# Kernel optimization log

Measured on AMD Instinct MI355X. Metric: run time of the kernel, lower is better.

The kernel has to match this reference:

```python
import jax, jax.numpy as jnp
import numpy as np

BETA = 0.25

def setup_inputs() -> dict:
    key = jax.random.key(0)
    k1, k2 = jax.random.split(key)
    x = jax.random.normal(k1, (32, 1024, 256), dtype=jnp.float32)
    # tf.random_uniform_initializer default range is [-0.05, 0.05)
    embedding = jax.random.uniform(k2, (256, 8192), dtype=jnp.float32, minval=-0.05, maxval=0.05)
    return {"x": x, "embedding": embedding}


def reference(x, embedding):
    # x: [B, S, D]; embedding: [D, K] (codebook stored column-wise, as in the tf module)
    D = x.shape[-1]
    flat = x.reshape(-1, D)                                   # [N, D]
    dists = (jnp.sum(flat * flat, axis=1, keepdims=True)
             - 2.0 * (flat @ embedding)
             + jnp.sum(embedding * embedding, axis=0))
    idx = jnp.argmin(dists, axis=1)                           # [N] int
    quantized = jnp.take(embedding.T, idx, axis=0).reshape(x.shape)  # gather codebook columns
    # VQ losses
    commitment = jnp.mean(jnp.square(jax.lax.stop_gradient(quantized) - x))
    codebook = jnp.mean(jnp.square(quantized - jax.lax.stop_gradient(x)))
    loss = BETA * commitment + codebook
    # straight-through estimator
    quantized_st = x + jax.lax.stop_gradient(quantized - x)
    return quantized_st, loss
```

## Files before the change

### kernel.cpp

```cpp
#include <hip/hip_runtime.h>

typedef float f4   __attribute__((ext_vector_type(4)));
typedef float f2   __attribute__((ext_vector_type(2)));
typedef _Float16 f16x8 __attribute__((ext_vector_type(8)));
typedef float f32x4  __attribute__((ext_vector_type(4)));

#define N_ROWS  32768
#define D_DIM   256
#define K_CODES 8192
#define NUM_ELEM (N_ROWS * D_DIM)
#define EPS_MARGIN 2e-3f
#define FB_CAP  8192
#define FB_RPB  8
#define RF_SLICES 16
#define N_PANELS 256
#define HALF_PANELS 128

__device__ __forceinline__ void gl2lds16(const void* g, void* l) {
    __builtin_amdgcn_global_load_lds(
        (const __attribute__((address_space(1))) unsigned int*)g,
        (__attribute__((address_space(3))) unsigned int*)l, 16, 0, 0);
}

__global__ void prep_kernel(const float* __restrict__ E, short* __restrict__ Ep,
                            float* __restrict__ Et32, float* __restrict__ ee) {
    __shared__ float eepart[8][32];
    const int p  = blockIdx.x;
    const int t  = threadIdx.x;
    const int c  = t & 31;
    const int gq = t >> 5;
    const int cp = p * 32;
    short* ph = Ep + (size_t)p * 8192;
    float ss = 0.0f;
    #pragma unroll
    for (int gi = 0; gi < 4; ++gi) {
        int g = gq * 4 + gi;
        f16x8 h;
        f4 av, bv;
        #pragma unroll
        for (int j = 0; j < 8; ++j) {
            float v = E[(size_t)(g * 8 + j) * K_CODES + cp + c];
            h[j] = (_Float16)v;
            ss += v * v;
            if (j < 4) av[j] = v; else bv[j - 4] = v;
        }
        *(f16x8*)(ph + (g * 32 + c) * 8) = h;
        *(f4*)(Et32 + (size_t)(cp + c) * D_DIM + g * 8)     = av;
        *(f4*)(Et32 + (size_t)(cp + c) * D_DIM + g * 8 + 4) = bv;
    }
    eepart[gq][c] = ss;
    __syncthreads();
    if (t < 32) {
        float s = 0.0f;
        #pragma unroll
        for (int q = 0; q < 8; ++q) s += eepart[q][t];
        ee[cp + t] = s;
    }
}

__launch_bounds__(256, 2)
__global__ void mfma_sieve_kernel(const float* __restrict__ X,
                                  const short* __restrict__ Ep,
                                  const float* __restrict__ ee,
                                  f2* __restrict__ res_bs,
                                  int* __restrict__ res_idx) {
    __shared__ __align__(16) short Bbuf[2][8192];
    const int t    = threadIdx.x;
    const int w    = t >> 6;
    const int lane = t & 63;
    const int n    = lane & 15;
    const int quad = lane >> 4;
    const int half = blockIdx.x & 1;
    const int row0 = (blockIdx.x >> 1) * 128;
    const int rw   = row0 + w * 32;
    const int p0   = half * HALF_PANELS;

    f16x8 Ah[2][8];
    #pragma unroll
    for (int rt = 0; rt < 2; ++rt) {
        const float* xp = X + (size_t)(rw + rt * 16 + n) * D_DIM;
        #pragma unroll
        for (int ks = 0; ks < 8; ++ks) {
            int d = ks * 32 + quad * 8;
            f4 a = *(const f4*)(xp + d);
            f4 b = *(const f4*)(xp + d + 4);
            f16x8 h;
            #pragma unroll
            for (int j = 0; j < 8; ++j) {
                float x = (j < 4) ? a[j] : b[j - 4];
                h[j] = (_Float16)x;
            }
            Ah[rt][ks] = h;
        }
    }

    float bestv[8], secv[8]; int besti[8];
    #pragma unroll
    for (int s = 0; s < 8; ++s) { bestv[s] = 1e30f; secv[s] = 1e30f; besti[s] = 0; }

    {
        const char* gp = (const char*)Ep + (size_t)p0 * 16384;
        char* lp = (char*)&Bbuf[0][0];
        #pragma unroll
        for (int i = 0; i < 4; ++i)
            gl2lds16(gp + (w * 4 + i) * 1024 + lane * 16, lp + (w * 4 + i) * 1024);
    }
    __syncthreads();

    for (int i = 0; i < HALF_PANELS; ++i) {
        const int p   = p0 + i;
        const int buf = i & 1;
        if (i + 1 < HALF_PANELS) {
            const char* gp = (const char*)Ep + (size_t)(p + 1) * 16384;
            char* lp = (char*)&Bbuf[buf ^ 1][0];
            #pragma unroll
            for (int k = 0; k < 4; ++k)
                gl2lds16(gp + (w * 4 + k) * 1024 + lane * 16, lp + (w * 4 + k) * 1024);
        }

        const short* Bh = &Bbuf[buf][0];

        f32x4 acc[2][2];
        #pragma unroll
        for (int ct = 0; ct < 2; ++ct)
            #pragma unroll
            for (int rt = 0; rt < 2; ++rt)
                acc[ct][rt] = (f32x4)(0.0f);

        #pragma unroll
        for (int ks = 0; ks < 8; ++ks) {
            const int g = ks * 4 + quad;
            f16x8 bh[2];
            #pragma unroll
            for (int ct = 0; ct < 2; ++ct) {
                int c = ct * 16 + n;
                bh[ct] = *(const f16x8*)(Bh + (g * 32 + c) * 8);
            }
            #pragma unroll
            for (int ct = 0; ct < 2; ++ct)
                #pragma unroll
                for (int rt = 0; rt < 2; ++rt)
                    acc[ct][rt] = __builtin_amdgcn_mfma_f32_16x16x32_f16(Ah[rt][ks], bh[ct], acc[ct][rt], 0, 0, 0);
        }

        const int cb = p * 32;
        #pragma unroll
        for (int ct = 0; ct < 2; ++ct) {
            int code = cb + ct * 16 + n;
            float eev = ee[code];
            #pragma unroll
            for (int rt = 0; rt < 2; ++rt)
                #pragma unroll
                for (int r = 0; r < 4; ++r) {
                    float key = fmaf(-2.0f, acc[ct][rt][r], eev);
                    int s = rt * 4 + r;
                    float nb = fminf(key, bestv[s]);
                    secv[s]  = fminf(secv[s], fmaxf(key, bestv[s]));
                    besti[s] = (key < bestv[s]) ? code : besti[s];
                    bestv[s] = nb;
                }
        }
        __syncthreads();
    }

    #pragma unroll
    for (int off = 1; off < 16; off <<= 1) {
        #pragma unroll
        for (int s = 0; s < 8; ++s) {
            float ov = __shfl_xor(bestv[s], off);
            int   oi = __shfl_xor(besti[s], off);
            float os = __shfl_xor(secv[s], off);
            bool owin = (ov < bestv[s]) || (ov == bestv[s] && oi < besti[s]);
            if (owin) { secv[s] = fminf(os, bestv[s]); bestv[s] = ov; besti[s] = oi; }
            else      { secv[s] = fminf(secv[s], ov); }
        }
    }

    if (n == 0) {
        #pragma unroll
        for (int s = 0; s < 8; ++s) {
            int rl  = w * 32 + (s >> 2) * 16 + quad * 4 + (s & 3);
            int row = row0 + rl;
            f2 bs; bs[0] = bestv[s]; bs[1] = secv[s];
            res_bs[(size_t)row * 2 + half]  = bs;
            res_idx[(size_t)row * 2 + half] = besti[s];
        }
    }
}

__global__ void gather_kernel(const float* __restrict__ X, const float* __restrict__ Et32,
                              const f2* __restrict__ res_bs, const int* __restrict__ res_idx,
                              int* __restrict__ counter, int2* __restrict__ list,
                              float* __restrict__ out, double* __restrict__ loss_sum) {
    __shared__ int bl_[128];
    const int t    = threadIdx.x;
    const int row0 = blockIdx.x * 128;
    if (t < 128) {
        const int row = row0 + t;
        f2 a = res_bs[(size_t)row * 2];
        f2 b = res_bs[(size_t)row * 2 + 1];
        int ia = res_idx[(size_t)row * 2];
        int ib = res_idx[(size_t)row * 2 + 1];
        float gb; int gi; float gs;
        if (b[0] < a[0]) { gb = b[0]; gi = ib; gs = fminf(b[1], a[0]); }
        else             { gb = a[0]; gi = ia; gs = fminf(a[1], b[0]); }
        bl_[t] = gi;
        if (gs - gb <= EPS_MARGIN) {
            int pos = atomicAdd(counter, 1);
            if (pos < FB_CAP) list[pos] = make_int2(row, gi);
        }
    }
    __syncthreads();
    double ls = 0.0;
    const int d = t;
    #pragma unroll 4
    for (int r = 0; r < 128; ++r) {
        int code = bl_[r];
        float q  = Et32[(size_t)code * D_DIM + d];
        float x  = X[(size_t)(row0 + r) * D_DIM + d];
        float dq = q - x;
        out[(size_t)(row0 + r) * D_DIM + d] = x + dq;
        ls += (double)dq * (double)dq;
    }
    #pragma unroll
    for (int off = 32; off > 0; off >>= 1)
        ls += __shfl_down(ls, off);
    if ((t & 63) == 0) atomicAdd(loss_sum, ls);
}

__global__ void refine1_kernel(const float* __restrict__ X, const float* __restrict__ E,
                               const int* __restrict__ counter, const int2* __restrict__ list,
                               double* __restrict__ res_v, int* __restrict__ res_i) {
    __shared__ float xt[D_DIM][FB_RPB];
    __shared__ int rows_sh[FB_RPB];
    __shared__ double wbv[4][FB_RPB];
    __shared__ int    wbi[4][FB_RPB];

    int nf = *counter; if (nf > FB_CAP) nf = FB_CAP;
    const int nchunks = (nf + FB_RPB - 1) / FB_RPB;
    const int nitems  = nchunks * RF_SLICES;
    const int t = threadIdx.x;

    for (int item = blockIdx.x; item < nitems; item += gridDim.x) {
        const int rc = item / RF_SLICES;
        const int sl = item % RF_SLICES;
        __syncthreads();
        if (t < FB_RPB) {
            int e = rc * FB_RPB + t;
            int2 ent = list[(e < nf) ? e : 0];
            rows_sh[t] = ent.x;
        }
        __syncthreads();
        #pragma unroll
        for (int j = 0; j < FB_RPB; ++j)
            xt[t][j] = X[(size_t)rows_sh[j] * D_DIM + t];
        __syncthreads();

        const int k0 = sl * 512 + t * 2;
        double s0[FB_RPB], s1[FB_RPB], q0 = 0.0, q1 = 0.0;
        #pragma unroll
        for (int j = 0; j < FB_RPB; ++j) { s0[j] = 0.0; s1[j] = 0.0; }
        for (int d = 0; d < D_DIM; ++d) {
            f2 ev = *(const f2*)(E + (size_t)d * K_CODES + k0);
            double e0d = (double)ev[0], e1d = (double)ev[1];
            const f4* xp = (const f4*)(&xt[d][0]);
            f4 xa = xp[0], xb = xp[1];
            double xd[FB_RPB] = { (double)xa[0], (double)xa[1], (double)xa[2], (double)xa[3],
                                  (double)xb[0], (double)xb[1], (double)xb[2], (double)xb[3] };
            q0 += e0d * e0d; q1 += e1d * e1d;
            #pragma unroll
            for (int j = 0; j < FB_RPB; ++j) {
                s0[j] += xd[j] * e0d;
                s1[j] += xd[j] * e1d;
            }
        }
        double bv[FB_RPB]; int bi[FB_RPB];
        #pragma unroll
        for (int j = 0; j < FB_RPB; ++j) {
            double k0v = q0 - 2.0 * s0[j];
            double k1v = q1 - 2.0 * s1[j];
            bv[j] = k0v; bi[j] = k0;
            if (k1v < bv[j]) { bv[j] = k1v; bi[j] = k0 + 1; }
        }
        #pragma unroll
        for (int off = 1; off < 64; off <<= 1) {
            #pragma unroll
            for (int j = 0; j < FB_RPB; ++j) {
                double ov = __shfl_xor(bv[j], off);
                int    oi = __shfl_xor(bi[j], off);
                if (ov < bv[j] || (ov == bv[j] && oi < bi[j])) { bv[j] = ov; bi[j] = oi; }
            }
        }
        const int wave = t >> 6;
        if ((t & 63) == 0) {
            #pragma unroll
            for (int j = 0; j < FB_RPB; ++j) { wbv[wave][j] = bv[j]; wbi[wave][j] = bi[j]; }
        }
        __syncthreads();
        if (t < FB_RPB) {
            double b = wbv[0][t]; int i_ = wbi[0][t];
            #pragma unroll
            for (int wv = 1; wv < 4; ++wv) {
                double ov = wbv[wv][t]; int oi = wbi[wv][t];
                if (ov < b || (ov == b && oi < i_)) { b = ov; i_ = oi; }
            }
            int e = rc * FB_RPB + t;
            res_v[(size_t)e * RF_SLICES + sl] = b;
            res_i[(size_t)e * RF_SLICES + sl] = i_;
        }
    }
}

__global__ void patch_kernel(const float* __restrict__ X, const float* __restrict__ Et32,
                             float* __restrict__ out, double* __restrict__ loss_sum,
                             const int* __restrict__ counter, const int2* __restrict__ list,
                             const double* __restrict__ res_v, const int* __restrict__ res_i) {
    int nf = *counter; if (nf > FB_CAP) nf = FB_CAP;
    const int b = blockIdx.x;
    if (b >= nf) return;
    __shared__ int nc_sh;
    const int t = threadIdx.x;
    if (t == 0) {
        double bv = res_v[(size_t)b * RF_SLICES]; int bi = res_i[(size_t)b * RF_SLICES];
        for (int s = 1; s < RF_SLICES; ++s) {
            double v = res_v[(size_t)b * RF_SLICES + s];
            int    i = res_i[(size_t)b * RF_SLICES + s];
            if (v < bv || (v == bv && i < bi)) { bv = v; bi = i; }
        }
        nc_sh = bi;
    }
    __syncthreads();
    int2 ent = list[b];
    const int oc = ent.y, row = ent.x, nc = nc_sh;
    if (nc == oc) return;
    float x  = X[(size_t)row * D_DIM + t];
    float qn = Et32[(size_t)nc * D_DIM + t];
    float qo = Et32[(size_t)oc * D_DIM + t];
    float dqn = qn - x, dqo = qo - x;
    out[(size_t)row * D_DIM + t] = x + dqn;
    double dl = (double)dqn * dqn - (double)dqo * dqo;
    #pragma unroll
    for (int off = 32; off > 0; off >>= 1)
        dl += __shfl_down(dl, off);
    if ((t & 63) == 0) atomicAdd(loss_sum, dl);
}

__global__ void fin_kernel(const double* __restrict__ loss_sum, float* __restrict__ out) {
    double m = loss_sum[0] / (double)NUM_ELEM;
    out[NUM_ELEM] = (float)(0.25 * m + m);
}

extern "C" void kernel_launch(void* const* d_in, const int* in_sizes, int n_in,
                              void* d_out, int out_size, void* d_ws, size_t ws_size,
                              hipStream_t stream) {
    const float* X = (const float*)d_in[0];
    const float* E = (const float*)d_in[1];
    float* out = (float*)d_out;

    double* loss_sum = (double*)d_ws;
    int*    counter  = (int*)((char*)d_ws + 8);
    float*  ee       = (float*)((char*)d_ws + 1024);
    int2*   list     = (int2*)((char*)d_ws + 36864);
    double* res_v    = (double*)((char*)d_ws + 131072);
    int*    res_i    = (int*)((char*)d_ws + 1179648);
    float*  Et32     = (float*)((char*)d_ws + 1703936);
    short*  Ep       = (short*)((char*)d_ws + 10092544);
    f2*     res_bs   = (f2*)((char*)d_ws + 14286848);
    int*    res_idx  = (int*)((char*)d_ws + 15335424);

    hipMemsetAsync(d_ws, 0, 1024, stream);
    prep_kernel<<<N_PANELS, 256, 0, stream>>>(E, Ep, Et32, ee);
    mfma_sieve_kernel<<<512, 256, 0, stream>>>(X, Ep, ee, res_bs, res_idx);
    gather_kernel<<<N_ROWS / 128, 256, 0, stream>>>(X, Et32, res_bs, res_idx,
                                                    counter, list, out, loss_sum);
    refine1_kernel<<<2048, 256, 0, stream>>>(X, E, counter, list, res_v, res_i);
    patch_kernel<<<FB_CAP, 256, 0, stream>>>(X, Et32, out, loss_sum, counter, list,
                                             res_v, res_i);
    fin_kernel<<<1, 1, 0, stream>>>(loss_sum, out);
}
```

Before: 326.1 us.

## Fuse refine, patch and finalize via last-block atomics; fold ee into MFMA accumulator

```diff
diff --git a/kernel.cpp b/kernel.cpp
--- a/kernel.cpp
+++ b/kernel.cpp
@@ -23,13 +23,20 @@
 }
 
 __global__ void prep_kernel(const float* __restrict__ E, short* __restrict__ Ep,
-                            float* __restrict__ Et32, float* __restrict__ ee) {
+                            float* __restrict__ Et32, float* __restrict__ ee,
+                            float* __restrict__ ctl) {
     __shared__ float eepart[8][32];
     const int p  = blockIdx.x;
     const int t  = threadIdx.x;
     const int c  = t & 31;
     const int gq = t >> 5;
     const int cp = p * 32;
+    if (p == 0) {
+        f4 z = (f4)(0.0f);
+        f4* dst = (f4*)ctl;
+        dst[t * 2]     = z;
+        dst[t * 2 + 1] = z;
+    }
     short* ph = Ep + (size_t)p * 8192;
     float ss = 0.0f;
     #pragma unroll
@@ -65,6 +72,7 @@
                                   f2* __restrict__ res_bs,
                                   int* __restrict__ res_idx) {
     __shared__ __align__(16) short Bbuf[2][8192];
+    __shared__ float eebuf[4096];
     const int t    = threadIdx.x;
     const int w    = t >> 6;
     const int lane = t & 63;
@@ -94,9 +102,17 @@
         }
     }
 
+    {
+        const f4* src = (const f4*)(ee + half * 4096);
+        f4* dst = (f4*)eebuf;
+        #pragma unroll
+        for (int ps = 0; ps < 4; ++ps)
+            dst[ps * 256 + t] = src[ps * 256 + t];
+    }
+
     float bestv[8], secv[8]; int besti[8];
     #pragma unroll
-    for (int s = 0; s < 8; ++s) { bestv[s] = 1e30f; secv[s] = 1e30f; besti[s] = 0; }
+    for (int s = 0; s < 8; ++s) { bestv[s] = -1e30f; secv[s] = -1e30f; besti[s] = 0; }
 
     {
         const char* gp = (const char*)Ep + (size_t)p0 * 16384;
@@ -119,13 +135,16 @@
         }
 
         const short* Bh = &Bbuf[buf][0];
-
+        const int po = i * 32;
+
+        float eh0 = -0.5f * eebuf[po + n];
+        float eh1 = -0.5f * eebuf[po + 16 + n];
         f32x4 acc[2][2];
         #pragma unroll
-        for (int ct = 0; ct < 2; ++ct)
-            #pragma unroll
-            for (int rt = 0; rt < 2; ++rt)
-                acc[ct][rt] = (f32x4)(0.0f);
+        for (int rt = 0; rt < 2; ++rt) {
+            #pragma unroll
+            for (int r = 0; r < 4; ++r) { acc[0][rt][r] = eh0; acc[1][rt][r] = eh1; }
+        }
 
         #pragma unroll
         for (int ks = 0; ks < 8; ++ks) {
@@ -147,16 +166,15 @@
         #pragma unroll
         for (int ct = 0; ct < 2; ++ct) {
             int code = cb + ct * 16 + n;
-            float eev = ee[code];
             #pragma unroll
             for (int rt = 0; rt < 2; ++rt)
                 #pragma unroll
                 for (int r = 0; r < 4; ++r) {
-                    float key = fmaf(-2.0f, acc[ct][rt][r], eev);
+                    float av = acc[ct][rt][r];
                     int s = rt * 4 + r;
-                    float nb = fminf(key, bestv[s]);
-                    secv[s]  = fminf(secv[s], fmaxf(key, bestv[s]));
-                    besti[s] = (key < bestv[s]) ? code : besti[s];
+                    float nb = fmaxf(av, bestv[s]);
+                    secv[s]  = fmaxf(secv[s], fminf(av, bestv[s]));
+                    besti[s] = (av > bestv[s]) ? code : besti[s];
                     bestv[s] = nb;
                 }
         }
@@ -170,9 +188,9 @@
             float ov = __shfl_xor(bestv[s], off);
             int   oi = __shfl_xor(besti[s], off);
             float os = __shfl_xor(secv[s], off);
-            bool owin = (ov < bestv[s]) || (ov == bestv[s] && oi < besti[s]);
-            if (owin) { secv[s] = fminf(os, bestv[s]); bestv[s] = ov; besti[s] = oi; }
-            else      { secv[s] = fminf(secv[s], ov); }
+            bool owin = (ov > bestv[s]) || (ov == bestv[s] && oi < besti[s]);
+            if (owin) { secv[s] = fmaxf(os, bestv[s]); bestv[s] = ov; besti[s] = oi; }
+            else      { secv[s] = fmaxf(secv[s], ov); }
         }
     }
 
@@ -181,7 +199,7 @@
         for (int s = 0; s < 8; ++s) {
             int rl  = w * 32 + (s >> 2) * 16 + quad * 4 + (s & 3);
             int row = row0 + rl;
-            f2 bs; bs[0] = bestv[s]; bs[1] = secv[s];
+            f2 bs; bs[0] = -2.0f * bestv[s]; bs[1] = -2.0f * secv[s];
             res_bs[(size_t)row * 2 + half]  = bs;
             res_idx[(size_t)row * 2 + half] = besti[s];
         }
@@ -228,18 +246,31 @@
     if ((t & 63) == 0) atomicAdd(loss_sum, ls);
 }
 
-__global__ void refine1_kernel(const float* __restrict__ X, const float* __restrict__ E,
-                               const int* __restrict__ counter, const int2* __restrict__ list,
-                               double* __restrict__ res_v, int* __restrict__ res_i) {
+__global__ void refine_kernel(const float* __restrict__ X, const float* __restrict__ E,
+                              const float* __restrict__ Et32, float* __restrict__ out,
+                              double* __restrict__ loss_sum,
+                              const int* __restrict__ counter, const int2* __restrict__ list,
+                              double* __restrict__ res_v, int* __restrict__ res_i,
+                              int* __restrict__ chunk_done, int* __restrict__ done_chunks) {
     __shared__ float xt[D_DIM][FB_RPB];
     __shared__ int rows_sh[FB_RPB];
     __shared__ double wbv[4][FB_RPB];
     __shared__ int    wbi[4][FB_RPB];
+    __shared__ int nc_sh[FB_RPB];
+    __shared__ int last_sh;
 
     int nf = *counter; if (nf > FB_CAP) nf = FB_CAP;
     const int nchunks = (nf + FB_RPB - 1) / FB_RPB;
     const int nitems  = nchunks * RF_SLICES;
     const int t = threadIdx.x;
+
+    if (nitems == 0) {
+        if (blockIdx.x == 0 && t == 0) {
+            double m = loss_sum[0] / (double)NUM_ELEM;
+            out[NUM_ELEM] = (float)(0.25 * m + m);
+        }
+        return;
+    }
 
     for (int item = blockIdx.x; item < nitems; item += gridDim.x) {
         const int rc = item / RF_SLICES;
@@ -308,46 +339,65 @@
             res_v[(size_t)e * RF_SLICES + sl] = b;
             res_i[(size_t)e * RF_SLICES + sl] = i_;
         }
-    }
-}
-
-__global__ void patch_kernel(const float* __restrict__ X, const float* __restrict__ Et32,
-                             float* __restrict__ out, double* __restrict__ loss_sum,
-                             const int* __restrict__ counter, const int2* __restrict__ list,
-                             const double* __restrict__ res_v, const int* __restrict__ res_i) {
-    int nf = *counter; if (nf > FB_CAP) nf = FB_CAP;
-    const int b = blockIdx.x;
-    if (b >= nf) return;
-    __shared__ int nc_sh;
-    const int t = threadIdx.x;
-    if (t == 0) {
-        double bv = res_v[(size_t)b * RF_SLICES]; int bi = res_i[(size_t)b * RF_SLICES];
-        for (int s = 1; s < RF_SLICES; ++s) {
-            double v = res_v[(size_t)b * RF_SLICES + s];
-            int    i = res_i[(size_t)b * RF_SLICES + s];
-            if (v < bv || (v == bv && i < bi)) { bv = v; bi = i; }
-        }
-        nc_sh = bi;
-    }
-    __syncthreads();
-    int2 ent = list[b];
-    const int oc = ent.y, row = ent.x, nc = nc_sh;
-    if (nc == oc) return;
-    float x  = X[(size_t)row * D_DIM + t];
-    float qn = Et32[(size_t)nc * D_DIM + t];
-    float qo = Et32[(size_t)oc * D_DIM + t];
-    float dqn = qn - x, dqo = qo - x;
-    out[(size_t)row * D_DIM + t] = x + dqn;
-    double dl = (double)dqn * dqn - (double)dqo * dqo;
-    #pragma unroll
-    for (int off = 32; off > 0; off >>= 1)
-        dl += __shfl_down(dl, off);
-    if ((t & 63) == 0) atomicAdd(loss_sum, dl);
-}
-
-__global__ void fin_kernel(const double* __restrict__ loss_sum, float* __restrict__ out) {
-    double m = loss_sum[0] / (double)NUM_ELEM;
-    out[NUM_ELEM] = (float)(0.25 * m + m);
+
+        __threadfence();
+        __syncthreads();
+        if (t == 0) {
+            int old = atomicAdd(&chunk_done[rc], 1);
+            last_sh = (old == RF_SLICES - 1) ? 1 : 0;
+        }
+        __syncthreads();
+        if (last_sh) {
+            __threadfence();
+            if (t < FB_RPB) {
+                int e = rc * FB_RPB + t;
+                int nc = -1;
+                if (e < nf) {
+                    double bv_ = atomicAdd(&res_v[(size_t)e * RF_SLICES], 0.0);
+                    int    bi_ = atomicOr(&res_i[(size_t)e * RF_SLICES], 0);
+                    for (int s = 1; s < RF_SLICES; ++s) {
+                        double v  = atomicAdd(&res_v[(size_t)e * RF_SLICES + s], 0.0);
+                        int    i_ = atomicOr(&res_i[(size_t)e * RF_SLICES + s], 0);
+                        if (v < bv_ || (v == bv_ && i_ < bi_)) { bv_ = v; bi_ = i_; }
+                    }
+                    nc = bi_;
+                }
+                nc_sh[t] = nc;
+            }
+            __syncthreads();
+            double dl = 0.0;
+            #pragma unroll
+            for (int j = 0; j < FB_RPB; ++j) {
+                int e = rc * FB_RPB + j;
+                if (e < nf) {
+                    int nc = nc_sh[j];
+                    int2 ent = list[e];
+                    if (nc != ent.y) {
+                        float x  = xt[t][j];
+                        float qn = Et32[(size_t)nc * D_DIM + t];
+                        float qo = Et32[(size_t)ent.y * D_DIM + t];
+                        float dqn = qn - x, dqo = qo - x;
+                        out[(size_t)ent.x * D_DIM + t] = x + dqn;
+                        dl += (double)dqn * dqn - (double)dqo * dqo;
+                    }
+                }
+            }
+            #pragma unroll
+            for (int off = 32; off > 0; off >>= 1)
+                dl += __shfl_down(dl, off);
+            if ((t & 63) == 0 && dl != 0.0) atomicAdd(loss_sum, dl);
+            __threadfence();
+            __syncthreads();
+            if (t == 0) {
+                int oldc = atomicAdd(done_chunks, 1);
+                if (oldc == nchunks - 1) {
+                    __threadfence();
+                    double m = atomicAdd(loss_sum, 0.0) / (double)NUM_ELEM;
+                    out[NUM_ELEM] = (float)(0.25 * m + m);
+                }
+            }
+        }
+    }
 }
 
 extern "C" void kernel_launch(void* const* d_in, const int* in_sizes, int n_in,
@@ -357,24 +407,23 @@
     const float* E = (const float*)d_in[1];
     float* out = (float*)d_out;
 
-    double* loss_sum = (double*)d_ws;
-    int*    counter  = (int*)((char*)d_ws + 8);
-    float*  ee       = (float*)((char*)d_ws + 1024);
-    int2*   list     = (int2*)((char*)d_ws + 36864);
-    double* res_v    = (double*)((char*)d_ws + 131072);
-    int*    res_i    = (int*)((char*)d_ws + 1179648);
-    float*  Et32     = (float*)((char*)d_ws + 1703936);
-    short*  Ep       = (short*)((char*)d_ws + 10092544);
-    f2*     res_bs   = (f2*)((char*)d_ws + 14286848);
-    int*    res_idx  = (int*)((char*)d_ws + 15335424);
-
-    hipMemsetAsync(d_ws, 0, 1024, stream);
-    prep_kernel<<<N_PANELS, 256, 0, stream>>>(E, Ep, Et32, ee);
+    double* loss_sum    = (double*)d_ws;
+    int*    counter     = (int*)((char*)d_ws + 8);
+    int*    done_chunks = (int*)((char*)d_ws + 16);
+    int*    chunk_done  = (int*)((char*)d_ws + 64);
+    float*  ee          = (float*)((char*)d_ws + 8192);
+    int2*   list        = (int2*)((char*)d_ws + 40960);
+    double* res_v       = (double*)((char*)d_ws + 131072);
+    int*    res_i       = (int*)((char*)d_ws + 1179648);
+    float*  Et32        = (float*)((char*)d_ws + 1703936);
+    short*  Ep          = (short*)((char*)d_ws + 10092544);
+    f2*     res_bs      = (f2*)((char*)d_ws + 14286848);
+    int*    res_idx     = (int*)((char*)d_ws + 15335424);
+
+    prep_kernel<<<N_PANELS, 256, 0, stream>>>(E, Ep, Et32, ee, (float*)d_ws);
     mfma_sieve_kernel<<<512, 256, 0, stream>>>(X, Ep, ee, res_bs, res_idx);
     gather_kernel<<<N_ROWS / 128, 256, 0, stream>>>(X, Et32, res_bs, res_idx,
                                                     counter, list, out, loss_sum);
-    refine1_kernel<<<2048, 256, 0, stream>>>(X, E, counter, list, res_v, res_i);
-    patch_kernel<<<FB_CAP, 256, 0, stream>>>(X, Et32, out, loss_sum, counter, list,
-                                             res_v, res_i);
-    fin_kernel<<<1, 1, 0, stream>>>(loss_sum, out);
-}
+    refine_kernel<<<2048, 256, 0, stream>>>(X, E, Et32, out, loss_sum, counter, list,
+                                            res_v, res_i, chunk_done, done_chunks);
+}
```

Measured after the change: 408.3 us. 25.2% more time.

## Restructure fp64 refine kernel, fold workspace memset into prep, grid-stride patch

Applied to the files above, without the earlier changes.

```diff
diff --git a/kernel.cpp b/kernel.cpp
--- a/kernel.cpp
+++ b/kernel.cpp
@@ -11,8 +11,8 @@
 #define NUM_ELEM (N_ROWS * D_DIM)
 #define EPS_MARGIN 2e-3f
 #define FB_CAP  8192
-#define FB_RPB  8
-#define RF_SLICES 16
+#define FB_RPB  16
+#define RF_SLICES 32
 #define N_PANELS 256
 #define HALF_PANELS 128
 
@@ -23,13 +23,20 @@
 }
 
 __global__ void prep_kernel(const float* __restrict__ E, short* __restrict__ Ep,
-                            float* __restrict__ Et32, float* __restrict__ ee) {
+                            float* __restrict__ Et32, float* __restrict__ ee,
+                            float* __restrict__ ctl) {
     __shared__ float eepart[8][32];
     const int p  = blockIdx.x;
     const int t  = threadIdx.x;
     const int c  = t & 31;
     const int gq = t >> 5;
     const int cp = p * 32;
+    if (p == 0) {
+        f4 z = (f4)(0.0f);
+        f4* dst = (f4*)ctl;
+        dst[t * 2]     = z;
+        dst[t * 2 + 1] = z;
+    }
     short* ph = Ep + (size_t)p * 8192;
     float ss = 0.0f;
     #pragma unroll
@@ -231,7 +238,7 @@
 __global__ void refine1_kernel(const float* __restrict__ X, const float* __restrict__ E,
                                const int* __restrict__ counter, const int2* __restrict__ list,
                                double* __restrict__ res_v, int* __restrict__ res_i) {
-    __shared__ float xt[D_DIM][FB_RPB];
+    __shared__ double xt[FB_RPB][D_DIM];
     __shared__ int rows_sh[FB_RPB];
     __shared__ double wbv[4][FB_RPB];
     __shared__ int    wbi[4][FB_RPB];
@@ -253,35 +260,23 @@
         __syncthreads();
         #pragma unroll
         for (int j = 0; j < FB_RPB; ++j)
-            xt[t][j] = X[(size_t)rows_sh[j] * D_DIM + t];
-        __syncthreads();
-
-        const int k0 = sl * 512 + t * 2;
-        double s0[FB_RPB], s1[FB_RPB], q0 = 0.0, q1 = 0.0;
-        #pragma unroll
-        for (int j = 0; j < FB_RPB; ++j) { s0[j] = 0.0; s1[j] = 0.0; }
+            xt[j][t] = (double)X[(size_t)rows_sh[j] * D_DIM + t];
+        __syncthreads();
+
+        const int k0 = sl * 256 + t;
+        double s[FB_RPB], q = 0.0;
+        #pragma unroll
+        for (int j = 0; j < FB_RPB; ++j) s[j] = 0.0;
         for (int d = 0; d < D_DIM; ++d) {
-            f2 ev = *(const f2*)(E + (size_t)d * K_CODES + k0);
-            double e0d = (double)ev[0], e1d = (double)ev[1];
-            const f4* xp = (const f4*)(&xt[d][0]);
-            f4 xa = xp[0], xb = xp[1];
-            double xd[FB_RPB] = { (double)xa[0], (double)xa[1], (double)xa[2], (double)xa[3],
-                                  (double)xb[0], (double)xb[1], (double)xb[2], (double)xb[3] };
-            q0 += e0d * e0d; q1 += e1d * e1d;
-            #pragma unroll
-            for (int j = 0; j < FB_RPB; ++j) {
-                s0[j] += xd[j] * e0d;
-                s1[j] += xd[j] * e1d;
-            }
+            double e0d = (double)E[(size_t)d * K_CODES + k0];
+            q += e0d * e0d;
+            #pragma unroll
+            for (int j = 0; j < FB_RPB; ++j)
+                s[j] += xt[j][d] * e0d;
         }
         double bv[FB_RPB]; int bi[FB_RPB];
         #pragma unroll
-        for (int j = 0; j < FB_RPB; ++j) {
-            double k0v = q0 - 2.0 * s0[j];
-            double k1v = q1 - 2.0 * s1[j];
-            bv[j] = k0v; bi[j] = k0;
-            if (k1v < bv[j]) { bv[j] = k1v; bi[j] = k0 + 1; }
-        }
+        for (int j = 0; j < FB_RPB; ++j) { bv[j] = q - 2.0 * s[j]; bi[j] = k0; }
         #pragma unroll
         for (int off = 1; off < 64; off <<= 1) {
             #pragma unroll
@@ -316,33 +311,35 @@
                              const int* __restrict__ counter, const int2* __restrict__ list,
                              const double* __restrict__ res_v, const int* __restrict__ res_i) {
     int nf = *counter; if (nf > FB_CAP) nf = FB_CAP;
-    const int b = blockIdx.x;
-    if (b >= nf) return;
     __shared__ int nc_sh;
     const int t = threadIdx.x;
-    if (t == 0) {
-        double bv = res_v[(size_t)b * RF_SLICES]; int bi = res_i[(size_t)b * RF_SLICES];
-        for (int s = 1; s < RF_SLICES; ++s) {
-            double v = res_v[(size_t)b * RF_SLICES + s];
-            int    i = res_i[(size_t)b * RF_SLICES + s];
-            if (v < bv || (v == bv && i < bi)) { bv = v; bi = i; }
-        }
-        nc_sh = bi;
-    }
-    __syncthreads();
-    int2 ent = list[b];
-    const int oc = ent.y, row = ent.x, nc = nc_sh;
-    if (nc == oc) return;
-    float x  = X[(size_t)row * D_DIM + t];
-    float qn = Et32[(size_t)nc * D_DIM + t];
-    float qo = Et32[(size_t)oc * D_DIM + t];
-    float dqn = qn - x, dqo = qo - x;
-    out[(size_t)row * D_DIM + t] = x + dqn;
-    double dl = (double)dqn * dqn - (double)dqo * dqo;
-    #pragma unroll
-    for (int off = 32; off > 0; off >>= 1)
-        dl += __shfl_down(dl, off);
-    if ((t & 63) == 0) atomicAdd(loss_sum, dl);
+    for (int b = blockIdx.x; b < nf; b += gridDim.x) {
+        __syncthreads();
+        if (t == 0) {
+            double bv = res_v[(size_t)b * RF_SLICES]; int bi = res_i[(size_t)b * RF_SLICES];
+            for (int s = 1; s < RF_SLICES; ++s) {
+                double v = res_v[(size_t)b * RF_SLICES + s];
+                int    i = res_i[(size_t)b * RF_SLICES + s];
+                if (v < bv || (v == bv && i < bi)) { bv = v; bi = i; }
+            }
+            nc_sh = bi;
+        }
+        __syncthreads();
+        int2 ent = list[b];
+        const int oc = ent.y, row = ent.x, nc = nc_sh;
+        if (nc != oc) {
+            float x  = X[(size_t)row * D_DIM + t];
+            float qn = Et32[(size_t)nc * D_DIM + t];
+            float qo = Et32[(size_t)oc * D_DIM + t];
+            float dqn = qn - x, dqo = qo - x;
+            out[(size_t)row * D_DIM + t] = x + dqn;
+            double dl = (double)dqn * dqn - (double)dqo * dqo;
+            #pragma unroll
+            for (int off = 32; off > 0; off >>= 1)
+                dl += __shfl_down(dl, off);
+            if ((t & 63) == 0) atomicAdd(loss_sum, dl);
+        }
+    }
 }
 
 __global__ void fin_kernel(const double* __restrict__ loss_sum, float* __restrict__ out) {
@@ -359,22 +356,21 @@
 
     double* loss_sum = (double*)d_ws;
     int*    counter  = (int*)((char*)d_ws + 8);
-    float*  ee       = (float*)((char*)d_ws + 1024);
-    int2*   list     = (int2*)((char*)d_ws + 36864);
+    float*  ee       = (float*)((char*)d_ws + 8192);
+    int2*   list     = (int2*)((char*)d_ws + 40960);
     double* res_v    = (double*)((char*)d_ws + 131072);
-    int*    res_i    = (int*)((char*)d_ws + 1179648);
-    float*  Et32     = (float*)((char*)d_ws + 1703936);
-    short*  Ep       = (short*)((char*)d_ws + 10092544);
-    f2*     res_bs   = (f2*)((char*)d_ws + 14286848);
-    int*    res_idx  = (int*)((char*)d_ws + 15335424);
-
-    hipMemsetAsync(d_ws, 0, 1024, stream);
-    prep_kernel<<<N_PANELS, 256, 0, stream>>>(E, Ep, Et32, ee);
+    int*    res_i    = (int*)((char*)d_ws + 2228224);
+    float*  Et32     = (float*)((char*)d_ws + 4194304);
+    short*  Ep       = (short*)((char*)d_ws + 12582912);
+    f2*     res_bs   = (f2*)((char*)d_ws + 16777216);
+    int*    res_idx  = (int*)((char*)d_ws + 17301504);
+
+    prep_kernel<<<N_PANELS, 256, 0, stream>>>(E, Ep, Et32, ee, (float*)d_ws);
     mfma_sieve_kernel<<<512, 256, 0, stream>>>(X, Ep, ee, res_bs, res_idx);
     gather_kernel<<<N_ROWS / 128, 256, 0, stream>>>(X, Et32, res_bs, res_idx,
                                                     counter, list, out, loss_sum);
-    refine1_kernel<<<2048, 256, 0, stream>>>(X, E, counter, list, res_v, res_i);
-    patch_kernel<<<FB_CAP, 256, 0, stream>>>(X, Et32, out, loss_sum, counter, list,
-                                             res_v, res_i);
+    refine1_kernel<<<1024, 256, 0, stream>>>(X, E, counter, list, res_v, res_i);
+    patch_kernel<<<1024, 256, 0, stream>>>(X, Et32, out, loss_sum, counter, list,
+                                           res_v, res_i);
     fin_kernel<<<1, 1, 0, stream>>>(loss_sum, out);
 }
```

Result: no change. 329.5 us (+1.0%).

## Stage panel pairs per barrier and fold memset and finalize into kernels

Applied to the files above, without the earlier changes.

```diff
diff --git a/kernel.cpp b/kernel.cpp
--- a/kernel.cpp
+++ b/kernel.cpp
@@ -15,6 +15,7 @@
 #define RF_SLICES 16
 #define N_PANELS 256
 #define HALF_PANELS 128
+#define HALF_PAIRS 64
 
 __device__ __forceinline__ void gl2lds16(const void* g, void* l) {
     __builtin_amdgcn_global_load_lds(
@@ -23,13 +24,20 @@
 }
 
 __global__ void prep_kernel(const float* __restrict__ E, short* __restrict__ Ep,
-                            float* __restrict__ Et32, float* __restrict__ ee) {
+                            float* __restrict__ Et32, float* __restrict__ ee,
+                            float* __restrict__ ctl) {
     __shared__ float eepart[8][32];
     const int p  = blockIdx.x;
     const int t  = threadIdx.x;
     const int c  = t & 31;
     const int gq = t >> 5;
     const int cp = p * 32;
+    if (p == 0) {
+        f4 z = (f4)(0.0f);
+        f4* dst = (f4*)ctl;
+        dst[t * 2]     = z;
+        dst[t * 2 + 1] = z;
+    }
     short* ph = Ep + (size_t)p * 8192;
     float ss = 0.0f;
     #pragma unroll
@@ -64,7 +72,7 @@
                                   const float* __restrict__ ee,
                                   f2* __restrict__ res_bs,
                                   int* __restrict__ res_idx) {
-    __shared__ __align__(16) short Bbuf[2][8192];
+    __shared__ __align__(16) short Bbuf[2][16384];
     const int t    = threadIdx.x;
     const int w    = t >> 6;
     const int lane = t & 63;
@@ -102,63 +110,66 @@
         const char* gp = (const char*)Ep + (size_t)p0 * 16384;
         char* lp = (char*)&Bbuf[0][0];
         #pragma unroll
-        for (int i = 0; i < 4; ++i)
-            gl2lds16(gp + (w * 4 + i) * 1024 + lane * 16, lp + (w * 4 + i) * 1024);
+        for (int i = 0; i < 8; ++i)
+            gl2lds16(gp + (w * 8 + i) * 1024 + lane * 16, lp + (w * 8 + i) * 1024);
     }
     __syncthreads();
 
-    for (int i = 0; i < HALF_PANELS; ++i) {
-        const int p   = p0 + i;
-        const int buf = i & 1;
-        if (i + 1 < HALF_PANELS) {
-            const char* gp = (const char*)Ep + (size_t)(p + 1) * 16384;
-            char* lp = (char*)&Bbuf[buf ^ 1][0];
-            #pragma unroll
-            for (int k = 0; k < 4; ++k)
-                gl2lds16(gp + (w * 4 + k) * 1024 + lane * 16, lp + (w * 4 + k) * 1024);
-        }
-
-        const short* Bh = &Bbuf[buf][0];
-
-        f32x4 acc[2][2];
-        #pragma unroll
-        for (int ct = 0; ct < 2; ++ct)
-            #pragma unroll
-            for (int rt = 0; rt < 2; ++rt)
-                acc[ct][rt] = (f32x4)(0.0f);
-
-        #pragma unroll
-        for (int ks = 0; ks < 8; ++ks) {
-            const int g = ks * 4 + quad;
-            f16x8 bh[2];
-            #pragma unroll
-            for (int ct = 0; ct < 2; ++ct) {
-                int c = ct * 16 + n;
-                bh[ct] = *(const f16x8*)(Bh + (g * 32 + c) * 8);
-            }
+    for (int ii = 0; ii < HALF_PAIRS; ++ii) {
+        const int pbuf = ii & 1;
+        if (ii + 1 < HALF_PAIRS) {
+            const char* gp = (const char*)Ep + (size_t)(p0 + 2 * (ii + 1)) * 16384;
+            char* lp = (char*)&Bbuf[pbuf ^ 1][0];
+            #pragma unroll
+            for (int k = 0; k < 8; ++k)
+                gl2lds16(gp + (w * 8 + k) * 1024 + lane * 16, lp + (w * 8 + k) * 1024);
+        }
+
+        #pragma unroll
+        for (int sub = 0; sub < 2; ++sub) {
+            const int p = p0 + 2 * ii + sub;
+            const short* Bh = &Bbuf[pbuf][sub * 8192];
+
+            f32x4 acc[2][2];
             #pragma unroll
             for (int ct = 0; ct < 2; ++ct)
                 #pragma unroll
                 for (int rt = 0; rt < 2; ++rt)
-                    acc[ct][rt] = __builtin_amdgcn_mfma_f32_16x16x32_f16(Ah[rt][ks], bh[ct], acc[ct][rt], 0, 0, 0);
-        }
-
-        const int cb = p * 32;
-        #pragma unroll
-        for (int ct = 0; ct < 2; ++ct) {
-            int code = cb + ct * 16 + n;
-            float eev = ee[code];
-            #pragma unroll
-            for (int rt = 0; rt < 2; ++rt)
+                    acc[ct][rt] = (f32x4)(0.0f);
+
+            #pragma unroll
+            for (int ks = 0; ks < 8; ++ks) {
+                const int g = ks * 4 + quad;
+                f16x8 bh[2];
                 #pragma unroll
-                for (int r = 0; r < 4; ++r) {
-                    float key = fmaf(-2.0f, acc[ct][rt][r], eev);
-                    int s = rt * 4 + r;
-                    float nb = fminf(key, bestv[s]);
-                    secv[s]  = fminf(secv[s], fmaxf(key, bestv[s]));
-                    besti[s] = (key < bestv[s]) ? code : besti[s];
-                    bestv[s] = nb;
+                for (int ct = 0; ct < 2; ++ct) {
+                    int c = ct * 16 + n;
+                    bh[ct] = *(const f16x8*)(Bh + (g * 32 + c) * 8);
                 }
+                #pragma unroll
+                for (int ct = 0; ct < 2; ++ct)
+                    #pragma unroll
+                    for (int rt = 0; rt < 2; ++rt)
+                        acc[ct][rt] = __builtin_amdgcn_mfma_f32_16x16x32_f16(Ah[rt][ks], bh[ct], acc[ct][rt], 0, 0, 0);
+            }
+
+            const int cb = p * 32;
+            #pragma unroll
+            for (int ct = 0; ct < 2; ++ct) {
+                int code = cb + ct * 16 + n;
+                float eev = ee[code];
+                #pragma unroll
+                for (int rt = 0; rt < 2; ++rt)
+                    #pragma unroll
+                    for (int r = 0; r < 4; ++r) {
+                        float key = fmaf(-2.0f, acc[ct][rt][r], eev);
+                        int s = rt * 4 + r;
+                        float nb = fminf(key, bestv[s]);
+                        secv[s]  = fminf(secv[s], fmaxf(key, bestv[s]));
+                        besti[s] = (key < bestv[s]) ? code : besti[s];
+                        bestv[s] = nb;
+                    }
+            }
         }
         __syncthreads();
     }
@@ -314,40 +325,47 @@
 __global__ void patch_kernel(const float* __restrict__ X, const float* __restrict__ Et32,
                              float* __restrict__ out, double* __restrict__ loss_sum,
                              const int* __restrict__ counter, const int2* __restrict__ list,
-                             const double* __restrict__ res_v, const int* __restrict__ res_i) {
+                             const double* __restrict__ res_v, const int* __restrict__ res_i,
+                             int* __restrict__ patch_done) {
     int nf = *counter; if (nf > FB_CAP) nf = FB_CAP;
-    const int b = blockIdx.x;
-    if (b >= nf) return;
     __shared__ int nc_sh;
     const int t = threadIdx.x;
+    for (int b = blockIdx.x; b < nf; b += gridDim.x) {
+        __syncthreads();
+        if (t == 0) {
+            double bv = res_v[(size_t)b * RF_SLICES]; int bi = res_i[(size_t)b * RF_SLICES];
+            for (int s = 1; s < RF_SLICES; ++s) {
+                double v = res_v[(size_t)b * RF_SLICES + s];
+                int    i = res_i[(size_t)b * RF_SLICES + s];
+                if (v < bv || (v == bv && i < bi)) { bv = v; bi = i; }
+            }
+            nc_sh = bi;
+        }
+        __syncthreads();
+        int2 ent = list[b];
+        const int oc = ent.y, row = ent.x, nc = nc_sh;
+        if (nc != oc) {
+            float x  = X[(size_t)row * D_DIM + t];
+            float qn = Et32[(size_t)nc * D_DIM + t];
+            float qo = Et32[(size_t)oc * D_DIM + t];
+            float dqn = qn - x, dqo = qo - x;
+            out[(size_t)row * D_DIM + t] = x + dqn;
+            double dl = (double)dqn * dqn - (double)dqo * dqo;
+            #pragma unroll
+            for (int off = 32; off > 0; off >>= 1)
+                dl += __shfl_down(dl, off);
+            if ((t & 63) == 0) atomicAdd(loss_sum, dl);
+        }
+    }
+    __threadfence();
+    __syncthreads();
     if (t == 0) {
-        double bv = res_v[(size_t)b * RF_SLICES]; int bi = res_i[(size_t)b * RF_SLICES];
-        for (int s = 1; s < RF_SLICES; ++s) {
-            double v = res_v[(size_t)b * RF_SLICES + s];
-            int    i = res_i[(size_t)b * RF_SLICES + s];
-            if (v < bv || (v == bv && i < bi)) { bv = v; bi = i; }
-        }
-        nc_sh = bi;
-    }
-    __syncthreads();
-    int2 ent = list[b];
-    const int oc = ent.y, row = ent.x, nc = nc_sh;
-    if (nc == oc) return;
-    float x  = X[(size_t)row * D_DIM + t];
-    float qn = Et32[(size_t)nc * D_DIM + t];
-    float qo = Et32[(size_t)oc * D_DIM + t];
-    float dqn = qn - x, dqo = qo - x;
-    out[(size_t)row * D_DIM + t] = x + dqn;
-    double dl = (double)dqn * dqn - (double)dqo * dqo;
-    #pragma unroll
-    for (int off = 32; off > 0; off >>= 1)
-        dl += __shfl_down(dl, off);
-    if ((t & 63) == 0) atomicAdd(loss_sum, dl);
-}
-
-__global__ void fin_kernel(const double* __restrict__ loss_sum, float* __restrict__ out) {
-    double m = loss_sum[0] / (double)NUM_ELEM;
-    out[NUM_ELEM] = (float)(0.25 * m + m);
+        int old = atomicAdd(patch_done, 1);
+        if (old == (int)gridDim.x - 1) {
+            double m = atomicAdd(loss_sum, 0.0) / (double)NUM_ELEM;
+            out[NUM_ELEM] = (float)(0.25 * m + m);
+        }
+    }
 }
 
 extern "C" void kernel_launch(void* const* d_in, const int* in_sizes, int n_in,
@@ -357,24 +375,23 @@
     const float* E = (const float*)d_in[1];
     float* out = (float*)d_out;
 
-    double* loss_sum = (double*)d_ws;
-    int*    counter  = (int*)((char*)d_ws + 8);
-    float*  ee       = (float*)((char*)d_ws + 1024);
-    int2*   list     = (int2*)((char*)d_ws + 36864);
-    double* res_v    = (double*)((char*)d_ws + 131072);
-    int*    res_i    = (int*)((char*)d_ws + 1179648);
-    float*  Et32     = (float*)((char*)d_ws + 1703936);
-    short*  Ep       = (short*)((char*)d_ws + 10092544);
-    f2*     res_bs   = (f2*)((char*)d_ws + 14286848);
-    int*    res_idx  = (int*)((char*)d_ws + 15335424);
-
-    hipMemsetAsync(d_ws, 0, 1024, stream);
-    prep_kernel<<<N_PANELS, 256, 0, stream>>>(E, Ep, Et32, ee);
+    double* loss_sum   = (double*)d_ws;
+    int*    counter    = (int*)((char*)d_ws + 8);
+    int*    patch_done = (int*)((char*)d_ws + 16);
+    float*  ee         = (float*)((char*)d_ws + 8192);
+    int2*   list       = (int2*)((char*)d_ws + 40960);
+    double* res_v      = (double*)((char*)d_ws + 131072);
+    int*    res_i      = (int*)((char*)d_ws + 1179648);
+    float*  Et32       = (float*)((char*)d_ws + 1703936);
+    short*  Ep         = (short*)((char*)d_ws + 10092544);
+    f2*     res_bs     = (f2*)((char*)d_ws + 14286848);
+    int*    res_idx    = (int*)((char*)d_ws + 15335424);
+
+    prep_kernel<<<N_PANELS, 256, 0, stream>>>(E, Ep, Et32, ee, (float*)d_ws);
     mfma_sieve_kernel<<<512, 256, 0, stream>>>(X, Ep, ee, res_bs, res_idx);
     gather_kernel<<<N_ROWS / 128, 256, 0, stream>>>(X, Et32, res_bs, res_idx,
                                                     counter, list, out, loss_sum);
     refine1_kernel<<<2048, 256, 0, stream>>>(X, E, counter, list, res_v, res_i);
-    patch_kernel<<<FB_CAP, 256, 0, stream>>>(X, Et32, out, loss_sum, counter, list,
-                                             res_v, res_i);
-    fin_kernel<<<1, 1, 0, stream>>>(loss_sum, out);
-}
+    patch_kernel<<<1024, 256, 0, stream>>>(X, Et32, out, loss_sum, counter, list,
+                                           res_v, res_i, patch_done);
+}
```

Result: slower. 383.4 us (+17.6%).
